# Optimization experiments

Measured on AMD Instinct MI355X. Metric: run time of the kernel, lower is better.

The kernel has to match this reference:

```python
import jax, jax.numpy as jnp
import numpy as np

C = 32           # in_channels
KH, KW = 3, 3    # kernel_range
SHIFT = 1
NP = KH * KW


def conv2d(x, w, b, pad):
    # x: NCHW, w: OIHW
    y = jax.lax.conv_general_dilated(
        x, w, window_strides=(1, 1), padding=[(pad, pad), (pad, pad)],
        dimension_numbers=('NCHW', 'OIHW', 'NCHW'))
    return y + b[None, :, None, None]


def setup_inputs() -> dict:
    key = jax.random.key(0)
    ks = jax.random.split(key, 14)
    p = lambda k, shape: (jax.random.normal(k, shape, dtype=jnp.float32) * 0.02)
    inp = {
        'x':  jax.random.normal(ks[0], (4, C, 256, 256), dtype=jnp.float32),
        'wk': p(ks[1], (C * NP, C, 1, 1)), 'bk': p(ks[2], (C * NP,)),
        'wv': p(ks[3], (C * NP, C, 1, 1)), 'bv': p(ks[4], (C * NP,)),
        'wq': p(ks[5], (C, C, 1, 1)),      'bq': p(ks[6], (C,)),
        'w1': p(ks[7], (C, C, 3, 3)),      'b1': p(ks[8], (C,)),
        'w2': p(ks[9], (2 * C, C, 3, 3)),  'b2': p(ks[10], (2 * C,)),
        'w3': p(ks[11], (C, 2 * C, 3, 3)), 'b3': p(ks[12], (C,)),
    }
    return inp


def reference(x, wk, bk, wv, bv, wq, bq, w1, b1, w2, b2, w3, b3):
    B, D, H, W = x.shape
    h_half, w_half = KH // 2, KW // 2
    ph, pw = h_half * SHIFT, w_half * SHIFT

    x_k = conv2d(x, wk, bk, 0)  # (B, D*NP, H, W)
    x_v = conv2d(x, wv, bv, 0)
    x_q = conv2d(x, wq, bq, 0)  # (B, D, H, W)

    pad4 = ((0, 0), (0, 0), (ph, ph), (pw, pw))
    x_k = jnp.pad(x_k, pad4)
    x_v = jnp.pad(x_v, pad4)
    mask_pad = jnp.pad(jnp.ones((B, 1, H, W), x.dtype), pad4)

    k_ls, v_ls, m_ls = [], [], []
    layer = 0
    for i in range(-h_half, h_half + 1):
        for j in range(-w_half, w_half + 1):
            r0 = ph + i * SHIFT
            c0 = pw + j * SHIFT
            k_ls.append(x_k[:, layer * D:(layer + 1) * D, r0:r0 + H, c0:c0 + W])
            v_ls.append(x_v[:, layer * D:(layer + 1) * D, r0:r0 + H, c0:c0 + W])
            m_ls.append(mask_pad[:, :, r0:r0 + H, c0:c0 + W])
            layer += 1

    # Faithful to torch .view semantics: flat row-major reshape, NOT a permute.
    k = jnp.stack(k_ls, axis=1).reshape(B * H * W, NP, D)   # (B,NP,D,H,W) -> flat
    v = jnp.stack(v_ls, axis=1).reshape(B * H * W, NP, D)
    m = jnp.stack(m_ls, axis=1).reshape(B * H * W, NP, 1)
    q = x_q.reshape(B * H * W, 1, D)                         # (B,D,H,W) -> flat

    scores = jnp.matmul(k, jnp.swapaxes(q, -1, -2)) * m / 8.0  # (N, NP, 1)
    alpha = jax.nn.softmax(scores, axis=1)
    res = jnp.matmul(jnp.swapaxes(alpha, -1, -2), v)           # (N, 1, D)
    t = res.reshape(B, D, H, W)

    t = jax.nn.relu(conv2d(t, w1, b1, 1))
    t = jax.nn.relu(conv2d(t, w2, b2, 1))
    t = jax.nn.relu(conv2d(t, w3, b3, 1))
    return t
```

## Files before the change

kernel.cpp:

```cpp
#include <hip/hip_runtime.h>
#include <hip/hip_bf16.h>

#define B_ 4
#define C_ 32
#define H_ 256
#define W_ 256
#define S_ 65536
#define NP_ 9
#define OC_ 288
#define PR 258
#define PWN 264

using bf16 = __hip_bfloat16;
typedef __attribute__((ext_vector_type(8)))  short  short8;
typedef __attribute__((ext_vector_type(4)))  short  short4_t;
typedef __attribute__((ext_vector_type(2)))  short  short2_t;
typedef __attribute__((ext_vector_type(16))) float  f32x16;

__device__ __forceinline__ float b2f(short s) {
    return __uint_as_float(((unsigned)(unsigned short)s) << 16);
}

template<int IC, int OC>
__device__ __forceinline__ void prepA_body(int fid, const float* __restrict__ w,
                                           bf16* __restrict__ apk)
{
    constexpr int NK = 9 * IC / 16;
    int tile = fid >> 9;
    int l = (fid >> 3) & 63;
    int j = fid & 7;
    int mt = tile / NK;
    int ks = tile - mt * NK;
    int q = l >> 5;
    int oc = mt * 32 + (l & 31);
    int k = ks * 16 + q * 8 + j;
    int tap = k / IC;
    int ic = k - tap * IC;
    apk[fid] = __float2bfloat16(w[((oc * IC + ic) * 3 + tap / 3) * 3 + tap % 3]);
}

template<int G>
__device__ __forceinline__ void zerob_body(int b, int p, uint4* __restrict__ buf)
{
    int gran;
    if (p < 2 * PWN * G) {
        int row = (p < PWN * G) ? 0 : 257;
        int rem = p % (PWN * G);
        gran = row * PWN * G + rem;
    } else {
        int p2 = p - 2 * PWN * G;
        int col = (p2 < 256 * G) ? 0 : 257;
        int rem = p2 % (256 * G);
        int r = rem / G + 1;
        int icg = rem - (rem / G) * G;
        gran = (r * PWN + col) * G + icg;
    }
    buf[(size_t)b * PR * PWN * G + gran] = uint4{0, 0, 0, 0};
}

__global__ __launch_bounds__(256) void k_prep(
    const float* __restrict__ wk, const float* __restrict__ wv,
    const float* __restrict__ wq,
    const float* __restrict__ w1, const float* __restrict__ w2,
    const float* __restrict__ w3,
    bf16* __restrict__ apk0, bf16* __restrict__ apk1,
    bf16* __restrict__ apk2, bf16* __restrict__ apk3,
    uint4* __restrict__ tA, uint4* __restrict__ t1, uint4* __restrict__ t2)
{
    int idx = blockIdx.x * 256 + threadIdx.x;
    if (idx < 19456) {
        int j    = idx & 7;
        int lane = (idx >> 3) & 63;
        int ks   = (idx >> 9) & 1;
        int mt   = idx >> 10;
        int oc = lane & 31;
        int ic = ks * 16 + (lane >> 5) * 8 + j;
        const float* w; int ocg;
        if (mt < 9)       { w = wk; ocg = mt * 32 + oc; }
        else if (mt < 18) { w = wv; ocg = (mt - 9) * 32 + oc; }
        else              { w = wq; ocg = oc; }
        apk0[idx] = __float2bfloat16(w[ocg * C_ + ic]);
    } else if (idx < 28672) {
        prepA_body<32, 32>(idx - 19456, w1, apk1);
    } else if (idx < 47104) {
        prepA_body<32, 64>(idx - 28672, w2, apk2);
    } else if (idx < 65536) {
        prepA_body<64, 32>(idx - 47104, w3, apk3);
    } else if (idx < 82176) {
        int i5 = idx - 65536;
        zerob_body<4>(i5 / 4160, i5 % 4160, tA);
    } else if (idx < 98816) {
        int i6 = idx - 82176;
        zerob_body<4>(i6 / 4160, i6 % 4160, t1);
    } else if (idx < 132096) {
        int i7 = idx - 98816;
        zerob_body<8>(i7 / 8320, i7 % 8320, t2);
    }
}

__global__ __launch_bounds__(256) void k_q(
    const float* __restrict__ x, const bf16* __restrict__ apk,
    const float* __restrict__ bq, bf16* __restrict__ xq)
{
    __shared__ bf16 lbuf[32][140];
    int bh  = blockIdx.x >> 9;
    int blk = blockIdx.x & 511;
    int pixw0 = blk << 7;
    int tid  = threadIdx.x;
    int wvi  = tid >> 6;
    int lane = tid & 63;
    int col  = lane & 31, q = lane >> 5;
    int pix  = pixw0 + wvi * 32 + col;

    const float* xb = x + (size_t)bh * (C_ * S_);
    bf16* xqb = xq + (size_t)bh * (32 * S_);

    short8 bfrag[2];
#pragma unroll
    for (int kk = 0; kk < 2; ++kk)
#pragma unroll
        for (int j = 0; j < 8; ++j) {
            bf16 h = __float2bfloat16(xb[(size_t)(kk * 16 + q * 8 + j) * S_ + pix]);
            bfrag[kk][j] = *reinterpret_cast<short*>(&h);
        }

    const short8* apkv = reinterpret_cast<const short8*>(apk);
    f32x16 acc = {};
    acc = __builtin_amdgcn_mfma_f32_32x32x16_bf16(bfrag[0], apkv[(18 * 2 + 0) * 64 + lane], acc, 0, 0, 0);
    acc = __builtin_amdgcn_mfma_f32_32x32x16_bf16(bfrag[1], apkv[(18 * 2 + 1) * 64 + lane], acc, 0, 0, 0);
    float bbv = bq[col];
#pragma unroll
    for (int g4 = 0; g4 < 4; ++g4) {
        short4_t sv;
#pragma unroll
        for (int j = 0; j < 4; ++j) {
            bf16 hb = __float2bfloat16(acc[g4 * 4 + j] + bbv);
            sv[j] = *reinterpret_cast<short*>(&hb);
        }
        *reinterpret_cast<short4_t*>(&lbuf[col][wvi * 32 + 8 * g4 + 4 * q]) = sv;
    }
    __syncthreads();
    int ch0 = tid >> 4, chk = tid & 15, ch1 = ch0 + 16;
    short8 v0 = *reinterpret_cast<const short8*>(&lbuf[ch0][chk * 8]);
    *reinterpret_cast<short8*>(xqb + (size_t)ch0 * S_ + pixw0 + chk * 8) = v0;
    short8 v1 = *reinterpret_cast<const short8*>(&lbuf[ch1][chk * 8]);
    *reinterpret_cast<short8*>(xqb + (size_t)ch1 * S_ + pixw0 + chk * 8) = v1;
}


__device__ __forceinline__ void tile_store(char* __restrict__ kvB, int T, int q, int oc,
                                           const f32x16& a, float bias,
                                           int dj, int hb_lo, int hb_hi)
{
#pragma unroll
    for (int G2 = 0; G2 < 4; ++G2) {
        int pxb = 32 * T + 8 * G2 + 4 * q;
        bool hbad = (pxb < hb_lo) || (pxb >= hb_hi);
        short4_t sv;
#pragma unroll
        for (int j3 = 0; j3 < 4; ++j3) {
            int px = pxb + j3;
            bool wbad = (dj == 1 && (px & 255) == 255) || (dj == -1 && (px & 255) == 0);
            float val = (hbad || wbad) ? 0.f : (a[G2 * 4 + j3] + bias);
            bf16 h = __float2bfloat16(val);
            sv[j3] = *reinterpret_cast<short*>(&h);
        }
        *reinterpret_cast<short4_t*>(kvB + oc * 1616 +
            (((T << 2) + (G2 ^ ((oc >> 3) & 3))) << 4) + q * 8) = sv;
    }
}

#define CONV_TILE(T, VH, COND)                                                        \
    VH = (f32x16){};                                                                  \
    if (COND) {                                                                       \
        int xib = 32 * (T) + 257 + di * 256 + dj + col;                               \
        int swx = (xib ^ (xib >> 2)) & 3;                                             \
        short8 fa = *reinterpret_cast<const short8*>(&xs[xib * 4 + (q ^ swx)]);       \
        short8 fb = *reinterpret_cast<const short8*>(&xs[xib * 4 + ((2 + q) ^ swx)]); \
        f32x16 ka = (f32x16){};                                                       \
        ka = __builtin_amdgcn_mfma_f32_32x32x16_bf16(fa, apkv[(p * 2 + 0) * 64 + lane], ka, 0, 0, 0); \
        ka = __builtin_amdgcn_mfma_f32_32x32x16_bf16(fb, apkv[(p * 2 + 1) * 64 + lane], ka, 0, 0, 0); \
        VH = __builtin_amdgcn_mfma_f32_32x32x16_bf16(fa, apkv[((9 + p) * 2 + 0) * 64 + lane], VH, 0, 0, 0); \
        VH = __builtin_amdgcn_mfma_f32_32x32x16_bf16(fb, apkv[((9 + p) * 2 + 1) * 64 + lane], VH, 0, 0, 0); \
        tile_store(kvB, (T), q, col, ka, bK, dj, hb_lo, hb_hi);                       \
    }

#define V_TILE(T, VH, COND)                                                           \
    if (COND) tile_store(kvB, (T), q, col, VH, bV, dj, hb_lo, hb_hi);

__global__ __launch_bounds__(1024, 4) void k_fused(
    const float* __restrict__ x,
    const bf16* __restrict__ apk,
    const float* __restrict__ bk, const float* __restrict__ bv,
    const bf16* __restrict__ xq,
    bf16* __restrict__ att)
{
    extern __shared__ char smem_raw[];
    uint4* xs  = reinterpret_cast<uint4*>(smem_raw);
    char*  kvB = smem_raw + 84096;

    int bb = blockIdx.x >> 7;
    int s0 = (blockIdx.x & 127) << 9;

    int tid  = threadIdx.x;
    int lane = tid & 63;
    int wv   = tid >> 6;
    int col  = lane & 31;
    int q    = lane >> 5;

    const float* xb = x + (size_t)bb * (C_ * S_);

    for (int i = tid; i < 5256; i += 1024) {
        int xi = i >> 2, g = i & 3;
        int s = s0 - 257 + xi;
        short8 v;
        if ((unsigned)s < 65536u) {
#pragma unroll
            for (int j = 0; j < 8; ++j) {
                bf16 h = __float2bfloat16(xb[(size_t)(g * 8 + j) * S_ + s]);
                v[j] = *reinterpret_cast<short*>(&h);
            }
        } else {
#pragma unroll
            for (int j = 0; j < 8; ++j) v[j] = 0;
        }
        int sw = (xi ^ (xi >> 2)) & 3;
        *reinterpret_cast<short8*>(&xs[xi * 4 + (g ^ sw)]) = v;
    }

    const short8* apkv = reinterpret_cast<const short8*>(apk);

    int grp  = tid >> 3, sub = tid & 7;
    int dp   = grp & 31;
    int krow = (grp >> 5) & 1;
    int hh   = sub >> 1;
    int sh   = sub & 1;
    bool athr = tid < 512;
    size_t qbase = ((size_t)bb << 21);

    __syncthreads();

#pragma unroll 1
    for (int p = 0; p < 9; ++p) {
        int di = p / 3 - 1, dj = p - (p / 3) * 3 - 1;
        int hb_lo = (di == -1) ? (256 - s0) : 0;
        int hb_hi = (di == 1) ? (65280 - s0) : 0x7FFFFFFF;
        float bK = bk[p * 32 + col];
        float bV = bv[p * 32 + col];

        int tl = 0, sk0 = 0; bool rv = false;
        short4_t qg = {};
        if (athr) {
            int plane_base = (p * 32 + dp) << 16;
            tl  = (plane_base + s0 + 287) / 288 + krow;
            sk0 = tl * 288 - plane_base;
            rv  = (sk0 < s0 + 512) && (sk0 <= 65248);
            if (rv) qg = *reinterpret_cast<const short4_t*>(
                         xq + qbase + ((size_t)tl << 5) + hh * 8 + sh * 4);
        }

        f32x16 vh0, vh1;
        CONV_TILE(wv,      vh0, true)
        CONV_TILE(wv + 16, vh1, (wv < 9))
        __syncthreads();

        float wgt[9];
        float inv_ = 0.f;
        if (rv) {
            float qv[4];
#pragma unroll
            for (int j = 0; j < 4; ++j) qv[j] = b2f(qg[j]);
            int swz = (dp >> 3) & 3;
            int t0  = (sk0 - s0) >> 5;
            float sc[9];
#pragma unroll
            for (int seg = 0; seg < 9; ++seg) {
                short4_t kg = *reinterpret_cast<const short4_t*>(
                    kvB + dp * 1616 + ((((t0 + seg) << 2) + (hh ^ swz)) << 4) + sh * 8);
                float dot = 0.f;
#pragma unroll
                for (int j = 0; j < 4; ++j) dot += qv[j] * b2f(kg[j]);
                dot += __shfl_xor(dot, 1);
                dot += __shfl_xor(dot, 2);
                dot += __shfl_xor(dot, 4);
                int rm = tl * 9 + seg;
                int pm = rm >> 16, sm = rm & 65535;
                int dim = pm / 3 - 1, djm = pm - (pm / 3) * 3 - 1;
                int hm = sm >> 8, wm = sm & 255;
                bool mval = ((unsigned)(hm + dim) < 256u) && ((unsigned)(wm + djm) < 256u);
                sc[seg] = mval ? dot * 0.125f : 0.f;
            }
            float mx = sc[0];
#pragma unroll
            for (int s2 = 1; s2 < 9; ++s2) mx = fmaxf(mx, sc[s2]);
            float sum = 0.f;
#pragma unroll
            for (int s2 = 0; s2 < 9; ++s2) { wgt[s2] = __expf(sc[s2] - mx); sum += wgt[s2]; }
            inv_ = 1.f / sum;
        }
        __syncthreads();

        V_TILE(wv,      vh0, true)
        V_TILE(wv + 16, vh1, (wv < 9))
        __syncthreads();

        if (rv) {
            int swz = (dp >> 3) & 3;
            int t0  = (sk0 - s0) >> 5;
            float oacc[4] = {0.f, 0.f, 0.f, 0.f};
#pragma unroll
            for (int seg = 0; seg < 9; ++seg) {
                short4_t vg = *reinterpret_cast<const short4_t*>(
                    kvB + dp * 1616 + ((((t0 + seg) << 2) + (hh ^ swz)) << 4) + sh * 8);
                float w_ = wgt[seg];
#pragma unroll
                for (int j = 0; j < 4; ++j) oacc[j] += w_ * b2f(vg[j]);
            }
            short4_t sv;
#pragma unroll
            for (int j = 0; j < 4; ++j) {
                bf16 h = __float2bfloat16(oacc[j] * inv_);
                sv[j] = *reinterpret_cast<short*>(&h);
            }
            *reinterpret_cast<short4_t*>(att + qbase + ((size_t)tl << 5) + hh * 8 + sh * 4) = sv;
        }
        __syncthreads();
    }
}

__global__ __launch_bounds__(320) void k_strad(
    const float* __restrict__ x,
    const float* __restrict__ wk, const float* __restrict__ bk,
    const float* __restrict__ wv, const float* __restrict__ bv,
    const bf16* __restrict__ xq, bf16* __restrict__ att)
{
    __shared__ float kL[288], vL[288], qL[32], wgtL[10];
    int e = blockIdx.x;
    int b = e >> 8, i = e & 255;
    int g = i >> 3, u = i & 7;
    int tl = g * 2048 + (((2040 + u) * 1593) & 2047);
    int tid = threadIdx.x;

    if (tid < 288) {
        int f  = tl * 288 + tid;
        int cp = f >> 16;
        int sp = f & 65535;
        int tap = cp >> 5;
        int di = tap / 3 - 1, dj = tap - (tap / 3) * 3 - 1;
        int h = sp >> 8, w = sp & 255;
        bool valid = ((unsigned)(h + di) < 256u) && ((unsigned)(w + dj) < 256u);
        float kv_ = 0.f, vv_ = 0.f;
        if (valid) {
            int sx = sp + di * 256 + dj;
            const float* xp = x + (size_t)b * (C_ * S_) + sx;
            float ks = bk[cp], vs = bv[cp];
#pragma unroll
            for (int ic = 0; ic < 32; ++ic) {
                float xv_ = xp[(size_t)ic * S_];
                ks += wk[cp * 32 + ic] * xv_;
                vs += wv[cp * 32 + ic] * xv_;
            }
            kv_ = ks; vv_ = vs;
        }
        kL[tid] = kv_; vL[tid] = vv_;
    }
    if (tid < 32) {
        bf16 hv = xq[(size_t)b * (32 * S_) + (size_t)tl * 32 + tid];
        qL[tid] = b2f(*reinterpret_cast<short*>(&hv));
    }
    __syncthreads();
    if (tid < 9) {
        float dot = 0.f;
#pragma unroll
        for (int d = 0; d < 32; ++d) dot += kL[tid * 32 + d] * qL[d];
        int rm = tl * 9 + tid;
        int pm = rm >> 16, sm = rm & 65535;
        int dim = pm / 3 - 1, djm = pm - (pm / 3) * 3 - 1;
        int hm = sm >> 8, wm = sm & 255;
        bool mval = ((unsigned)(hm + dim) < 256u) && ((unsigned)(wm + djm) < 256u);
        wgtL[tid] = mval ? dot * 0.125f : 0.f;
    }
    __syncthreads();
    if (tid == 0) {
        float mx = wgtL[0];
#pragma unroll
        for (int s2 = 1; s2 < 9; ++s2) mx = fmaxf(mx, wgtL[s2]);
        float sum = 0.f;
#pragma unroll
        for (int s2 = 0; s2 < 9; ++s2) { wgtL[s2] = __expf(wgtL[s2] - mx); sum += wgtL[s2]; }
        wgtL[9] = 1.f / sum;
    }
    __syncthreads();
    if (tid < 32) {
        float acc = 0.f;
#pragma unroll
        for (int seg = 0; seg < 9; ++seg) acc += wgtL[seg] * vL[seg * 32 + tid];
        att[(size_t)b * 2097152 + (size_t)tl * 32 + tid] = __float2bfloat16(acc * wgtL[9]);
    }
}

__global__ __launch_bounds__(256) void k_repack(
    const bf16* __restrict__ att, bf16* __restrict__ tA)
{
    int idx = blockIdx.x * 256 + threadIdx.x;
    int icg = idx & 3;
    int ps  = idx >> 2;
    int b = ps >> 16;
    int s = ps & 65535;
    const bf16* src = att + (size_t)b * (32 * S_) + icg * 8 * S_ + s;
    short8 v;
#pragma unroll
    for (int j = 0; j < 8; ++j)
        v[j] = *reinterpret_cast<const short*>(src + (size_t)j * S_);
    int row = (s >> 8) + 1, colp = (s & 255) + 1;
    *reinterpret_cast<short8*>(tA + ((size_t)((b * PR + row) * PWN + colp)) * 32 + icg * 8) = v;
}

template<int IC, int OC, bool NCHW_OUT>
__global__ __launch_bounds__(256) void k_conv3s(
    const bf16* __restrict__ in,
    const bf16* __restrict__ apk,
    const float* __restrict__ bs,
    void* __restrict__ outv)
{
    constexpr int G    = IC / 8;
    constexpr int M    = OC / 32;
    constexpr int KPT  = IC / 16;
    constexpr int NK   = 9 * KPT;
    constexpr int NT   = 2;
    constexpr int ROWP = 66;
    constexpr int ROWG = ROWP * G;
    constexpr int TOTG = 6 * ROWG;

    __shared__ uint4 smem[TOTG];

    int wg   = blockIdx.x;
    int orig = (wg & 7) * 128 + (wg >> 3);
    int b   = orig >> 8;
    int rem = orig & 255;
    int h0  = (rem >> 2) << 2;
    int w0  = (rem & 3) * 64;

    int tid = threadIdx.x;

    {
        const uint4* src = reinterpret_cast<const uint4*>(in);
#pragma unroll
        for (int i = 0; i < (TOTG + 255) / 256; ++i) {
            int idx = tid + i * 256;
            if (idx < TOTG) {
                int dr = idx / ROWG;
                int r2 = idx - dr * ROWG;
                uint4 v = src[((size_t)(b * PR + h0 + dr) * PWN + w0) * G + r2];
                int px = r2 >> ((G == 4) ? 2 : 3);
                int sw = (G == 4) ? ((px ^ (px >> 2)) & 3) : (px & 7);
                smem[dr * ROWG + (r2 & ~(G - 1)) + ((r2 ^ sw) & (G - 1))] = v;
            }
        }
    }
    __syncthreads();

    int lane = tid & 63;
    int wid  = tid >> 6;
    int col  = lane & 31, q = lane >> 5;
    int h    = h0 + wid;

    const short8* apkv = reinterpret_cast<const short8*>(apk);

    f32x16 acc[NT][M];
#pragma unroll
    for (int nt = 0; nt < NT; ++nt)
#pragma unroll
        for (int mt = 0; mt < M; ++mt) acc[nt][mt] = (f32x16){};

#pragma unroll
    for (int tap = 0; tap < 9; ++tap) {
        int dr = tap / 3 + wid;
        int dj = tap % 3;
#pragma unroll
        for (int icq = 0; icq < KPT; ++icq) {
            short8 bfr[NT];
#pragma unroll
            for (int nt = 0; nt < NT; ++nt) {
                int px = nt * 32 + col + dj;
                int sw = (G == 4) ? ((px ^ (px >> 2)) & 3) : (px & 7);
                bfr[nt] = *reinterpret_cast<const short8*>(
                    &smem[dr * ROWG + px * G + ((icq * 2 + q) ^ sw)]);
            }
#pragma unroll
            for (int mt = 0; mt < M; ++mt) {
                short8 afr = apkv[(mt * NK + tap * KPT + icq) * 64 + lane];
#pragma unroll
                for (int nt = 0; nt < NT; ++nt)
                    acc[nt][mt] = __builtin_amdgcn_mfma_f32_32x32x16_bf16(
                        afr, bfr[nt], acc[nt][mt], 0, 0, 0);
            }
        }
    }

#pragma unroll
    for (int nt = 0; nt < NT; ++nt) {
        int wout = w0 + nt * 32 + col;
#pragma unroll
        for (int mt = 0; mt < M; ++mt) {
            if (NCHW_OUT) {
                float* out = (float*)outv;
#pragma unroll
                for (int r = 0; r < 16; ++r) {
                    int oc = mt * 32 + (r & 3) + 8 * (r >> 2) + 4 * q;
                    out[(size_t)((b * OC + oc) * H_ + h) * W_ + wout] =
                        fmaxf(acc[nt][mt][r] + bs[oc], 0.f);
                }
            } else {
                bf16* out = (bf16*)outv;
                size_t base = (size_t)((b * PR + h + 1) * PWN + wout + 1) * OC + mt * 32 + 4 * q;
#pragma unroll
                for (int g4 = 0; g4 < 4; ++g4) {
                    short4_t sv;
#pragma unroll
                    for (int r4 = 0; r4 < 4; ++r4) {
                        int oc = mt * 32 + 8 * g4 + 4 * q + r4;
                        bf16 hh = __float2bfloat16(fmaxf(acc[nt][mt][g4 * 4 + r4] + bs[oc], 0.f));
                        sv[r4] = *reinterpret_cast<short*>(&hh);
                    }
                    *reinterpret_cast<short4_t*>(out + base + 8 * g4) = sv;
                }
            }
        }
    }
}

extern "C" void kernel_launch(void* const* d_in, const int* in_sizes, int n_in,
                              void* d_out, int out_size, void* d_ws, size_t ws_size,
                              hipStream_t stream)
{
    const float* x  = (const float*)d_in[0];
    const float* wk = (const float*)d_in[1];
    const float* bk = (const float*)d_in[2];
    const float* wv = (const float*)d_in[3];
    const float* bv = (const float*)d_in[4];
    const float* wq = (const float*)d_in[5];
    const float* bq = (const float*)d_in[6];
    const float* w1 = (const float*)d_in[7];
    const float* b1 = (const float*)d_in[8];
    const float* w2 = (const float*)d_in[9];
    const float* b2 = (const float*)d_in[10];
    const float* w3 = (const float*)d_in[11];
    const float* b3 = (const float*)d_in[12];
    float* out = (float*)d_out;
    char* ws = (char*)d_ws;

    bf16* xq   = (bf16*)(ws);
    bf16* tA   = (bf16*)(ws + 16777216);
    bf16* t1   = (bf16*)(ws + 34213888);
    bf16* t2   = (bf16*)(ws + 51650560);
    bf16* apk0 = (bf16*)(ws + 86523904);
    bf16* apk1 = (bf16*)(ws + 86562816);
    bf16* apk2 = (bf16*)(ws + 86581248);
    bf16* apk3 = (bf16*)(ws + 86618112);
    bf16* attB = (bf16*)d_out;

    static bool attr_set = false;
    if (!attr_set) {
        hipFuncSetAttribute(reinterpret_cast<const void*>(k_fused),
                            hipFuncAttributeMaxDynamicSharedMemorySize, 135808);
        attr_set = true;
    }

    k_prep<<<516, 256, 0, stream>>>(wk, wv, wq, w1, w2, w3,
                                    apk0, apk1, apk2, apk3,
                                    (uint4*)tA, (uint4*)t1, (uint4*)t2);

    k_q<<<2048, 256, 0, stream>>>(x, apk0, bq, xq);

    k_fused<<<512, 1024, 135808, stream>>>(x, apk0, bk, bv, xq, attB);

    k_strad<<<1024, 320, 0, stream>>>(x, wk, bk, wv, bv, xq, attB);

    k_repack<<<4096, 256, 0, stream>>>(attB, tA);

    k_conv3s<32, 32, false><<<1024, 256, 0, stream>>>(tA, apk1, b1, (void*)t1);
    k_conv3s<32, 64, false><<<1024, 256, 0, stream>>>(t1, apk2, b2, (void*)t2);
    k_conv3s<64, 32, true ><<<1024, 256, 0, stream>>>(t2, apk3, b3, (void*)out);
}
```

Before: 182.8 us.

## Fuse K score dot-product into conv epilogue, keep only V in LDS

The K projection tile is no longer written to shared memory. Each conv tile's K accumulator is dotted directly against the matching query vector loaded from global memory. The per-row scores go into a small LDS score array, and only V is stored to the kv buffer. This removes one shared-memory K store and load pass and two barriers per kernel offset, at the cost of extra global query loads per tile, slightly more LDS, and more complex boundary masking.

```diff
diff --git a/kernel.cpp b/kernel.cpp
--- a/kernel.cpp
+++ b/kernel.cpp
@@ -14,7 +14,6 @@
 using bf16 = __hip_bfloat16;
 typedef __attribute__((ext_vector_type(8)))  short  short8;
 typedef __attribute__((ext_vector_type(4)))  short  short4_t;
-typedef __attribute__((ext_vector_type(2)))  short  short2_t;
 typedef __attribute__((ext_vector_type(16))) float  f32x16;
 
 __device__ __forceinline__ float b2f(short s) {
@@ -148,45 +147,56 @@
 }
 
 
-__device__ __forceinline__ void tile_store(char* __restrict__ kvB, int T, int q, int oc,
-                                           const f32x16& a, float bias,
-                                           int dj, int hb_lo, int hb_hi)
-{
-#pragma unroll
-    for (int G2 = 0; G2 < 4; ++G2) {
-        int pxb = 32 * T + 8 * G2 + 4 * q;
-        bool hbad = (pxb < hb_lo) || (pxb >= hb_hi);
-        short4_t sv;
-#pragma unroll
-        for (int j3 = 0; j3 < 4; ++j3) {
-            int px = pxb + j3;
-            bool wbad = (dj == 1 && (px & 255) == 255) || (dj == -1 && (px & 255) == 0);
-            float val = (hbad || wbad) ? 0.f : (a[G2 * 4 + j3] + bias);
-            bf16 h = __float2bfloat16(val);
-            sv[j3] = *reinterpret_cast<short*>(&h);
-        }
-        *reinterpret_cast<short4_t*>(kvB + oc * 1616 +
-            (((T << 2) + (G2 ^ ((oc >> 3) & 3))) << 4) + q * 8) = sv;
-    }
-}
-
-#define CONV_TILE(T, VH, COND)                                                        \
-    VH = (f32x16){};                                                                  \
-    if (COND) {                                                                       \
-        int xib = 32 * (T) + 257 + di * 256 + dj + col;                               \
-        int swx = (xib ^ (xib >> 2)) & 3;                                             \
-        short8 fa = *reinterpret_cast<const short8*>(&xs[xib * 4 + (q ^ swx)]);       \
-        short8 fb = *reinterpret_cast<const short8*>(&xs[xib * 4 + ((2 + q) ^ swx)]); \
-        f32x16 ka = (f32x16){};                                                       \
-        ka = __builtin_amdgcn_mfma_f32_32x32x16_bf16(fa, apkv[(p * 2 + 0) * 64 + lane], ka, 0, 0, 0); \
-        ka = __builtin_amdgcn_mfma_f32_32x32x16_bf16(fb, apkv[(p * 2 + 1) * 64 + lane], ka, 0, 0, 0); \
-        VH = __builtin_amdgcn_mfma_f32_32x32x16_bf16(fa, apkv[((9 + p) * 2 + 0) * 64 + lane], VH, 0, 0, 0); \
-        VH = __builtin_amdgcn_mfma_f32_32x32x16_bf16(fb, apkv[((9 + p) * 2 + 1) * 64 + lane], VH, 0, 0, 0); \
-        tile_store(kvB, (T), q, col, ka, bK, dj, hb_lo, hb_hi);                       \
-    }
-
-#define V_TILE(T, VH, COND)                                                           \
-    if (COND) tile_store(kvB, (T), q, col, VH, bV, dj, hb_lo, hb_hi);
+#define DO_TILE(T, DTOT)                                                              \
+{                                                                                     \
+    int Tg = (s0 >> 5) + (T);                                                         \
+    unsigned n = (unsigned)plane_base + ((unsigned)Tg << 5);                          \
+    unsigned tl = (n >> 5) / 9u;                               \
+    int sk0 = (int)(tl * 288u) - plane_base;                                          \
+    const bf16* qp = xqb + ((size_t)tl << 5) + 4 * q;                                 \
+    short4_t q0 = *reinterpret_cast<const short4_t*>(qp);                             \
+    short4_t q1 = *reinterpret_cast<const short4_t*>(qp + 8);                         \
+    short4_t q2 = *reinterpret_cast<const short4_t*>(qp + 16);                        \
+    short4_t q3 = *reinterpret_cast<const short4_t*>(qp + 24);                        \
+    int xib = ((T) << 5) + 257 + di * 256 + dj + col;                                 \
+    int swx = (xib ^ (xib >> 2)) & 3;                                                 \
+    short8 fa = *reinterpret_cast<const short8*>(&xs[xib * 4 + (q ^ swx)]);           \
+    short8 fb = *reinterpret_cast<const short8*>(&xs[xib * 4 + ((2 + q) ^ swx)]);     \
+    f32x16 ka = (f32x16){}, vh = (f32x16){};                                          \
+    ka = __builtin_amdgcn_mfma_f32_32x32x16_bf16(fa, apkv[(p * 2 + 0) * 64 + lane], ka, 0, 0, 0); \
+    ka = __builtin_amdgcn_mfma_f32_32x32x16_bf16(fb, apkv[(p * 2 + 1) * 64 + lane], ka, 0, 0, 0); \
+    vh = __builtin_amdgcn_mfma_f32_32x32x16_bf16(fa, apkv[((9 + p) * 2 + 0) * 64 + lane], vh, 0, 0, 0); \
+    vh = __builtin_amdgcn_mfma_f32_32x32x16_bf16(fb, apkv[((9 + p) * 2 + 1) * 64 + lane], vh, 0, 0, 0); \
+    bool hbad  = (32 * (T) < hb_lo) || (32 * (T) >= hb_hi);                           \
+    bool tb_lo = (dj == -1) && ((Tg & 7) == 0);                                       \
+    bool tb_hi = (dj == 1) && ((Tg & 7) == 7);                                        \
+    if (tb_lo && q == 0) q0[0] = 0;                       \
+    if (tb_hi && q == 1) q3[3] = 0;                      \
+    float dot = 0.f;                                                                  \
+    _Pragma("unroll")                                                                 \
+    for (int j3 = 0; j3 < 4; ++j3) {                                                  \
+        dot += (ka[j3]      + bK) * b2f(q0[j3]);                                      \
+        dot += (ka[4 + j3]  + bK) * b2f(q1[j3]);                                      \
+        dot += (ka[8 + j3]  + bK) * b2f(q2[j3]);                                      \
+        dot += (ka[12 + j3] + bK) * b2f(q3[j3]);                                      \
+    }                                                                                 \
+    if (hbad) dot = 0.f;                                                              \
+    DTOT = dot + __shfl_xor(dot, 32);                                                 \
+    _Pragma("unroll")                                                                 \
+    for (int G2 = 0; G2 < 4; ++G2) {                                                  \
+        short4_t sv;                                                                  \
+        _Pragma("unroll")                                                             \
+        for (int j3 = 0; j3 < 4; ++j3) {                                              \
+            float val = hbad ? 0.f : (vh[G2 * 4 + j3] + bV);                          \
+            bf16 hcv = __float2bfloat16(val);                                         \
+            sv[j3] = *reinterpret_cast<short*>(&hcv);                                 \
+        }                                                                             \
+        if (G2 == 0 && tb_lo && q == 0) sv[0] = 0;                                    \
+        if (G2 == 3 && tb_hi && q == 1) sv[3] = 0;                                    \
+        *reinterpret_cast<short4_t*>(kvB + col * 1616 +                               \
+            ((((T) << 2) + (G2 ^ ((col >> 3) & 3))) << 4) + q * 8) = sv;              \
+    }                                                                                 \
+}
 
 __global__ __launch_bounds__(1024, 4) void k_fused(
     const float* __restrict__ x,
@@ -198,6 +208,7 @@
     extern __shared__ char smem_raw[];
     uint4* xs  = reinterpret_cast<uint4*>(smem_raw);
     char*  kvB = smem_raw + 84096;
+    float* scL = reinterpret_cast<float*>(smem_raw + 135808);
 
     int bb = blockIdx.x >> 7;
     int s0 = (blockIdx.x & 127) << 9;
@@ -209,6 +220,8 @@
     int q    = lane >> 5;
 
     const float* xb = x + (size_t)bb * (C_ * S_);
+    size_t qbase = ((size_t)bb << 21);
+    const bf16* xqb = xq + qbase;
 
     for (int i = tid; i < 5256; i += 1024) {
         int xi = i >> 2, g = i & 3;
@@ -236,93 +249,71 @@
     int hh   = sub >> 1;
     int sh   = sub & 1;
     bool athr = tid < 512;
-    size_t qbase = ((size_t)bb << 21);
 
     __syncthreads();
 
 #pragma unroll 1
     for (int p = 0; p < 9; ++p) {
         int di = p / 3 - 1, dj = p - (p / 3) * 3 - 1;
-        int hb_lo = (di == -1) ? (256 - s0) : 0;
-        int hb_hi = (di == 1) ? (65280 - s0) : 0x7FFFFFFF;
+        int hb_lo = (di == -1) ? (256 - s0) : (-0x40000000);
+        int hb_hi = (di == 1) ? (65280 - s0) : 0x40000000;
         float bK = bk[p * 32 + col];
         float bV = bv[p * 32 + col];
-
-        int tl = 0, sk0 = 0; bool rv = false;
-        short4_t qg = {};
+        int plane_base = (p * 32 + col) << 16;
+
+        float dA, dB = 0.f;
+        DO_TILE(wv, dA)
+        if (wv < 9) { DO_TILE(wv + 16, dB) }
+
+        if (q == 0)      scL[wv * 32 + col] = dA;
+        else if (wv < 9) scL[(wv + 16) * 32 + col] = dB;
+        __syncthreads();
+
         if (athr) {
-            int plane_base = (p * 32 + dp) << 16;
-            tl  = (plane_base + s0 + 287) / 288 + krow;
-            sk0 = tl * 288 - plane_base;
-            rv  = (sk0 < s0 + 512) && (sk0 <= 65248);
-            if (rv) qg = *reinterpret_cast<const short4_t*>(
-                         xq + qbase + ((size_t)tl << 5) + hh * 8 + sh * 4);
-        }
-
-        f32x16 vh0, vh1;
-        CONV_TILE(wv,      vh0, true)
-        CONV_TILE(wv + 16, vh1, (wv < 9))
-        __syncthreads();
-
-        float wgt[9];
-        float inv_ = 0.f;
-        if (rv) {
-            float qv[4];
-#pragma unroll
-            for (int j = 0; j < 4; ++j) qv[j] = b2f(qg[j]);
-            int swz = (dp >> 3) & 3;
-            int t0  = (sk0 - s0) >> 5;
-            float sc[9];
-#pragma unroll
-            for (int seg = 0; seg < 9; ++seg) {
-                short4_t kg = *reinterpret_cast<const short4_t*>(
-                    kvB + dp * 1616 + ((((t0 + seg) << 2) + (hh ^ swz)) << 4) + sh * 8);
-                float dot = 0.f;
-#pragma unroll
-                for (int j = 0; j < 4; ++j) dot += qv[j] * b2f(kg[j]);
-                dot += __shfl_xor(dot, 1);
-                dot += __shfl_xor(dot, 2);
-                dot += __shfl_xor(dot, 4);
-                int rm = tl * 9 + seg;
-                int pm = rm >> 16, sm = rm & 65535;
-                int dim = pm / 3 - 1, djm = pm - (pm / 3) * 3 - 1;
-                int hm = sm >> 8, wm = sm & 255;
-                bool mval = ((unsigned)(hm + dim) < 256u) && ((unsigned)(wm + djm) < 256u);
-                sc[seg] = mval ? dot * 0.125f : 0.f;
-            }
-            float mx = sc[0];
-#pragma unroll
-            for (int s2 = 1; s2 < 9; ++s2) mx = fmaxf(mx, sc[s2]);
-            float sum = 0.f;
-#pragma unroll
-            for (int s2 = 0; s2 < 9; ++s2) { wgt[s2] = __expf(sc[s2] - mx); sum += wgt[s2]; }
-            inv_ = 1.f / sum;
-        }
-        __syncthreads();
-
-        V_TILE(wv,      vh0, true)
-        V_TILE(wv + 16, vh1, (wv < 9))
-        __syncthreads();
-
-        if (rv) {
-            int swz = (dp >> 3) & 3;
-            int t0  = (sk0 - s0) >> 5;
-            float oacc[4] = {0.f, 0.f, 0.f, 0.f};
-#pragma unroll
-            for (int seg = 0; seg < 9; ++seg) {
-                short4_t vg = *reinterpret_cast<const short4_t*>(
-                    kvB + dp * 1616 + ((((t0 + seg) << 2) + (hh ^ swz)) << 4) + sh * 8);
-                float w_ = wgt[seg];
-#pragma unroll
-                for (int j = 0; j < 4; ++j) oacc[j] += w_ * b2f(vg[j]);
-            }
-            short4_t sv;
-#pragma unroll
-            for (int j = 0; j < 4; ++j) {
-                bf16 h = __float2bfloat16(oacc[j] * inv_);
-                sv[j] = *reinterpret_cast<short*>(&h);
-            }
-            *reinterpret_cast<short4_t*>(att + qbase + ((size_t)tl << 5) + hh * 8 + sh * 4) = sv;
+            int plane_base_r = (p * 32 + dp) << 16;
+            unsigned tl = ((unsigned)(plane_base_r + s0 + 287)) / 288u + (unsigned)krow;
+            int sk0 = (int)(tl * 288u) - plane_base_r;
+            bool rv = (sk0 < s0 + 512) && (sk0 <= 65248);
+            if (rv) {
+                int t0  = (sk0 - s0) >> 5;
+                int swz = (dp >> 3) & 3;
+                float sc[9];
+#pragma unroll
+                for (int seg = 0; seg < 9; ++seg) {
+                    float d = scL[(t0 + seg) * 32 + dp];
+                    int rm = (int)tl * 9 + seg;
+                    int pm = rm >> 16, sm = rm & 65535;
+                    int dim = pm / 3 - 1, djm = pm - (pm / 3) * 3 - 1;
+                    int hm = sm >> 8, wm = sm & 255;
+                    bool mval = ((unsigned)(hm + dim) < 256u) && ((unsigned)(wm + djm) < 256u);
+                    sc[seg] = mval ? d * 0.125f : 0.f;
+                }
+                float mx = sc[0];
+#pragma unroll
+                for (int s2 = 1; s2 < 9; ++s2) mx = fmaxf(mx, sc[s2]);
+                float wgt[9];
+                float sum = 0.f;
+#pragma unroll
+                for (int s2 = 0; s2 < 9; ++s2) { wgt[s2] = __expf(sc[s2] - mx); sum += wgt[s2]; }
+                float inv_ = 1.f / sum;
+
+                float oacc[4] = {0.f, 0.f, 0.f, 0.f};
+#pragma unroll
+                for (int seg = 0; seg < 9; ++seg) {
+                    short4_t vg = *reinterpret_cast<const short4_t*>(
+                        kvB + dp * 1616 + ((((t0 + seg) << 2) + (hh ^ swz)) << 4) + sh * 8);
+                    float w_ = wgt[seg];
+#pragma unroll
+                    for (int j = 0; j < 4; ++j) oacc[j] += w_ * b2f(vg[j]);
+                }
+                short4_t sv;
+#pragma unroll
+                for (int j = 0; j < 4; ++j) {
+                    bf16 h = __float2bfloat16(oacc[j] * inv_);
+                    sv[j] = *reinterpret_cast<short*>(&h);
+                }
+                *reinterpret_cast<short4_t*>(att + qbase + ((size_t)tl << 5) + hh * 8 + sh * 4) = sv;
+            }
         }
         __syncthreads();
     }
@@ -563,7 +554,7 @@
     static bool attr_set = false;
     if (!attr_set) {
         hipFuncSetAttribute(reinterpret_cast<const void*>(k_fused),
-                            hipFuncAttributeMaxDynamicSharedMemorySize, 135808);
+                            hipFuncAttributeMaxDynamicSharedMemorySize, 139008);
         attr_set = true;
     }
 
@@ -573,7 +564,7 @@
 
     k_q<<<2048, 256, 0, stream>>>(x, apk0, bq, xq);
 
-    k_fused<<<512, 1024, 135808, stream>>>(x, apk0, bk, bv, xq, attB);
+    k_fused<<<512, 1024, 139008, stream>>>(x, apk0, bk, bv, xq, attB);
 
     k_strad<<<1024, 320, 0, stream>>>(x, wk, bk, wv, bv, xq, attB);
 
```

New measurement: 187.0 us. 2.3% more time.
